# Optimization experiments

Hardware: AMD Instinct MI355X
Metric: run time of the kernel (lower is better)

## Reference

```python
import jax, jax.numpy as jnp
import numpy as np

H = 2048        # hidden_size
NH = 16         # query heads
NKV = 4         # kv heads (= NH//4, from k_proj shape H x H//4)
HD = H // NH    # head_dim = 128
B, S = 2, 2048
SCALE = 1.0 / (HD ** 0.5)


def _rope(x, cos, sin):
    # x: [B, h, S, d]; cos/sin: [S, d//2]; rotate complex pairs (even, odd)
    xr = x[..., 0::2]
    xi = x[..., 1::2]
    c = cos[None, None, :x.shape[2], :]
    s = sin[None, None, :x.shape[2], :]
    out_r = xr * c - xi * s
    out_i = xr * s + xi * c
    return jnp.stack([out_r, out_i], axis=-1).reshape(x.shape)


def setup_inputs() -> dict:
    key = jax.random.key(0)
    ks = jax.random.split(key, 6)
    hidden_states = jax.random.normal(ks[0], (B, S, H), dtype=jnp.float32)
    # RoPE table (theta = 10000), head_dim//2 frequencies
    inv_freq = 1.0 / (10000.0 ** (np.arange(0, HD, 2, dtype=np.float32) / HD))
    angles = np.arange(S, dtype=np.float32)[:, None] * inv_freq[None, :]
    freqs_cos = jnp.asarray(np.cos(angles), dtype=jnp.float32)
    freqs_sin = jnp.asarray(np.sin(angles), dtype=jnp.float32)
    w = 0.02  # keep activations in a sane range
    Wq = jax.random.normal(ks[1], (H, H), dtype=jnp.float32) * w
    Wk = jax.random.normal(ks[2], (H // 4, H), dtype=jnp.float32) * w
    Wv = jax.random.normal(ks[3], (H // 4, H), dtype=jnp.float32) * w
    Wo = jax.random.normal(ks[4], (H, H), dtype=jnp.float32) * w
    return {"hidden_states": hidden_states, "freqs_cos": freqs_cos,
            "freqs_sin": freqs_sin, "Wq": Wq, "Wk": Wk, "Wv": Wv, "Wo": Wo}


def reference(hidden_states, freqs_cos, freqs_sin, Wq, Wk, Wv, Wo):
    b, s, _ = hidden_states.shape
    q = hidden_states @ Wq.T                      # [B,S,H]
    k = hidden_states @ Wk.T                      # [B,S,H/4]
    v = hidden_states @ Wv.T                      # [B,S,H/4]
    q = q.reshape(b, s, NH, HD).transpose(0, 2, 1, 3)    # [B,NH,S,HD]
    k = k.reshape(b, s, NKV, HD).transpose(0, 2, 1, 3)   # [B,NKV,S,HD]
    v = v.reshape(b, s, NKV, HD).transpose(0, 2, 1, 3)
    q = _rope(q, freqs_cos, freqs_sin)
    k = _rope(k, freqs_cos, freqs_sin)
    # GQA: each kv head serves NH//NKV query heads
    k_rep = jnp.repeat(k, NH // NKV, axis=1)      # [B,NH,S,HD]
    v_rep = jnp.repeat(v, NH // NKV, axis=1)
    scores = jnp.einsum('bhqd,bhkd->bhqk', q, k_rep) * SCALE  # [B,NH,S,S]
    probs = jax.nn.softmax(scores, axis=-1)
    out = jnp.einsum('bhqk,bhkd->bhqd', probs, v_rep)         # [B,NH,S,HD]
    out = out.transpose(0, 2, 1, 3).reshape(b, s, H)
    return out @ Wo.T
```

## Files before the change

kernel.cpp:

```cpp
#include <hip/hip_runtime.h>

typedef __bf16 bf16_t;
typedef bf16_t bf16x8 __attribute__((ext_vector_type(8)));
typedef bf16_t bf16x4 __attribute__((ext_vector_type(4)));
typedef bf16_t bf16x2 __attribute__((ext_vector_type(2)));
typedef float f32x4 __attribute__((ext_vector_type(4)));
typedef float f32x16 __attribute__((ext_vector_type(16)));
typedef unsigned int u32x4 __attribute__((ext_vector_type(4)));

typedef const __attribute__((address_space(1))) void* as1_cvp;
typedef __attribute__((address_space(3))) void* as3_vp;

__device__ __forceinline__ void gload16(const void* g, void* l) {
  __builtin_amdgcn_global_load_lds((as1_cvp)g, (as3_vp)l, 16, 0, 0);
}

__device__ __forceinline__ unsigned pxor32(unsigned x) {
  return (unsigned)__shfl_xor((int)x, 32);
}

__global__ __launch_bounds__(256) void cvt_kernel(const float* __restrict__ src,
                                                  bf16_t* __restrict__ dst, int n8) {
  int i = blockIdx.x * 256 + threadIdx.x;
  if (i >= n8) return;
  int idx = i * 8;
  float4 a = *(const float4*)(src + idx);
  float4 b = *(const float4*)(src + idx + 4);
  bf16x8 o;
  o[0] = (bf16_t)a.x; o[1] = (bf16_t)a.y; o[2] = (bf16_t)a.z; o[3] = (bf16_t)a.w;
  o[4] = (bf16_t)b.x; o[5] = (bf16_t)b.y; o[6] = (bf16_t)b.z; o[7] = (bf16_t)b.w;
  *(bf16x8*)(dst + idx) = o;
}

#define BM 128
#define BN 128
#define BK 64

__global__ __launch_bounds__(256, 2) void gemm_bt(const bf16_t* __restrict__ A,
                                                  const bf16_t* __restrict__ B,
                                                  float* __restrict__ C,
                                                  int M, int N, int K) {
  __shared__ alignas(16) bf16_t As[BM * BK];
  __shared__ alignas(16) bf16_t Bs[BN * BK];
  const int t = threadIdx.x;
  const int lane = t & 63, w = t >> 6;
  const int wm = w >> 1, wn = w & 1;
  const int lr = lane & 15, lg = lane >> 4;
  const int m0 = blockIdx.y * BM, n0 = blockIdx.x * BN;
  const int srow = t >> 3, scol = (t & 7) * 8;

  f32x4 acc[4][4] = {};

  for (int kb = 0; kb < K; kb += BK) {
    __syncthreads();
#pragma unroll
    for (int i = 0; i < 4; ++i) {
      gload16(A + (size_t)(m0 + srow + 32 * i) * K + kb + scol, As + i * 2048 + t * 8);
      gload16(B + (size_t)(n0 + srow + 32 * i) * K + kb + scol, Bs + i * 2048 + t * 8);
    }
    __syncthreads();
#pragma unroll
    for (int kk = 0; kk < 2; ++kk) {
      const int ko = kk * 32 + lg * 8;
      bf16x8 af[4], bfr[4];
#pragma unroll
      for (int r = 0; r < 4; ++r)
        af[r] = *(const bf16x8*)(As + (wm * 64 + r * 16 + lr) * BK + ko);
#pragma unroll
      for (int c = 0; c < 4; ++c)
        bfr[c] = *(const bf16x8*)(Bs + (wn * 64 + c * 16 + lr) * BK + ko);
#pragma unroll
      for (int r = 0; r < 4; ++r)
#pragma unroll
        for (int c = 0; c < 4; ++c)
          acc[r][c] = __builtin_amdgcn_mfma_f32_16x16x32_bf16(af[r], bfr[c], acc[r][c], 0, 0, 0);
    }
  }
#pragma unroll
  for (int r = 0; r < 4; ++r)
#pragma unroll
    for (int c = 0; c < 4; ++c)
#pragma unroll
      for (int b = 0; b < 4; ++b)
        C[(size_t)(m0 + wm * 64 + r * 16 + lg * 4 + b) * N + n0 + wn * 64 + c * 16 + lr] =
            acc[r][c][b];
}

__global__ __launch_bounds__(256, 2) void gemm_qkv(const bf16_t* __restrict__ A,
                                                   const bf16_t* __restrict__ B,
                                                   const float* __restrict__ cs,
                                                   const float* __restrict__ sn,
                                                   bf16_t* __restrict__ qr,
                                                   bf16_t* __restrict__ kr,
                                                   bf16_t* __restrict__ vt) {
  __shared__ alignas(16) bf16_t As[BM * BK];
  __shared__ alignas(16) bf16_t Bs[BN * BK];
  const int K = 2048;
  const int t = threadIdx.x;
  const int lane = t & 63, w = t >> 6;
  const int wm = w >> 1, wn = w & 1;
  const int lr = lane & 15, lg = lane >> 4;
  const int m0 = blockIdx.y * BM, n0 = blockIdx.x * BN;
  const int srow = t >> 3, scol = (t & 7) * 8;

  f32x4 acc[4][4] = {};

  for (int kb = 0; kb < K; kb += BK) {
    __syncthreads();
#pragma unroll
    for (int i = 0; i < 4; ++i) {
      gload16(A + (size_t)(m0 + srow + 32 * i) * K + kb + scol, As + i * 2048 + t * 8);
      gload16(B + (size_t)(n0 + srow + 32 * i) * K + kb + scol, Bs + i * 2048 + t * 8);
    }
    __syncthreads();
#pragma unroll
    for (int kk = 0; kk < 2; ++kk) {
      const int ko = kk * 32 + lg * 8;
      bf16x8 af[4], bfr[4];
#pragma unroll
      for (int r = 0; r < 4; ++r)
        af[r] = *(const bf16x8*)(As + (wm * 64 + r * 16 + lr) * BK + ko);
#pragma unroll
      for (int c = 0; c < 4; ++c)
        bfr[c] = *(const bf16x8*)(Bs + (wn * 64 + c * 16 + lr) * BK + ko);
#pragma unroll
      for (int r = 0; r < 4; ++r)
#pragma unroll
        for (int c = 0; c < 4; ++c)
          acc[r][c] = __builtin_amdgcn_mfma_f32_16x16x32_bf16(af[r], bfr[c], acc[r][c], 0, 0, 0);
    }
  }

  const int head = n0 >> 7;
  const int bb2 = m0 >> 11;
  const int sbase = (m0 & 2047) + wm * 64 + lg * 4;
  if (head < 20) {
    bf16_t* dst = (head < 16) ? qr + (size_t)(bb2 * 16 + head) * 2048 * 128
                              : kr + (size_t)(bb2 * 4 + (head - 16)) * 2048 * 128;
    const bool evn = (lr & 1) == 0;
#pragma unroll
    for (int r = 0; r < 4; ++r)
#pragma unroll
      for (int c = 0; c < 4; ++c) {
        const int cw = wn * 64 + c * 16 + lr;
        const int dix = cw >> 1;
#pragma unroll
        for (int b = 0; b < 4; ++b) {
          const int s = sbase + r * 16 + b;
          float own = acc[r][c][b];
          float prt = __shfl_xor(own, 1);
          if (evn) {
            float cc = cs[s * 64 + dix];
            float ssn = sn[s * 64 + dix];
            bf16x2 pr;
            pr[0] = (bf16_t)(own * cc - prt * ssn);
            pr[1] = (bf16_t)(own * ssn + prt * cc);
            *(bf16x2*)(dst + (size_t)s * 128 + cw) = pr;
          }
        }
      }
  } else {
    bf16_t* dst = vt + (size_t)(bb2 * 4 + (head - 20)) * 128 * 2048;
#pragma unroll
    for (int r = 0; r < 4; ++r)
#pragma unroll
      for (int c = 0; c < 4; ++c) {
        const int cw = wn * 64 + c * 16 + lr;
        const int s = sbase + r * 16;
        bf16x4 v4;
#pragma unroll
        for (int b = 0; b < 4; ++b) v4[b] = (bf16_t)acc[r][c][b];
        *(bf16x4*)(dst + (size_t)cw * 2048 + s) = v4;
      }
  }
}

#define KVB 64
__global__ __launch_bounds__(256, 2) void attn_kernel(const bf16_t* __restrict__ Q,
                                                      const bf16_t* __restrict__ Kg,
                                                      const bf16_t* __restrict__ Vg,
                                                      bf16_t* __restrict__ O) {
  __shared__ alignas(16) bf16_t Ks[2][16 * KVB * 8];
  __shared__ alignas(16) bf16_t Vs[8 * 128 * 8];
  const int t = threadIdx.x;
  const int lane = t & 63, w = t >> 6;
  const int l31 = lane & 31, hi = lane >> 5;
  const int bid = ((blockIdx.x & 7) << 6) | (blockIdx.x >> 3);
  const int qt = bid & 15;
  const int h = (bid >> 4) & 15;
  const int bb = bid >> 8;
  const int kvh = h >> 2;

  const bf16_t* Qh = Q + (((size_t)bb * 16 + h) * 2048 + qt * 128 + w * 32) * 128;
  const bf16_t* Kh = Kg + ((size_t)bb * 4 + kvh) * 2048 * 128;
  const bf16_t* Vh = Vg + ((size_t)bb * 4 + kvh) * 128 * 2048;

  bf16x8 qf[8];
#pragma unroll
  for (int c = 0; c < 8; ++c)
    qf[c] = *(const bf16x8*)(Qh + l31 * 128 + c * 16 + hi * 8);

  f32x16 o[4] = {};
  float m2 = -1e30f;
  float ls = 0.f;
  const float sm = 0.08838834764831845f * 1.44269504088896f;

#define STAGE_K(buf, kb)                                                                \
  _Pragma("unroll") for (int i = 0; i < 4; ++i)                                         \
    gload16(Kh + (size_t)((kb) + (t & 63)) * 128 + (i * 4 + (t >> 6)) * 8,              \
            &Ks[buf][(i * 256 + t) * 8]);
#define STAGE_V(kb)                                                                     \
  _Pragma("unroll") for (int i = 0; i < 4; ++i)                                         \
    gload16(Vh + (size_t)(t & 127) * 2048 + (kb) + (i * 2 + (t >> 7)) * 8,              \
            &Vs[(i * 256 + t) * 8]);

  STAGE_K(0, 0);
  __syncthreads();

  for (int tt = 0; tt < 32; ++tt) {
    const int cur = tt & 1;
    STAGE_V(tt * KVB);
    if (tt < 31) { STAGE_K(cur ^ 1, (tt + 1) * KVB); }
    const bf16_t* Kc = Ks[cur];

    f32x16 s0 = {}, s1 = {};
    __builtin_amdgcn_s_setprio(1);
#pragma unroll
    for (int c = 0; c < 8; ++c) {
      bf16x8 kf0 = *(const bf16x8*)(Kc + ((c * 2 + hi) * 64 + l31) * 8);
      bf16x8 kf1 = *(const bf16x8*)(Kc + ((c * 2 + hi) * 64 + 32 + l31) * 8);
      s0 = __builtin_amdgcn_mfma_f32_32x32x16_bf16(kf0, qf[c], s0, 0, 0, 0);
      s1 = __builtin_amdgcn_mfma_f32_32x32x16_bf16(kf1, qf[c], s1, 0, 0, 0);
    }
    __builtin_amdgcn_s_setprio(0);
    s0 = s0 * sm;
    s1 = s1 * sm;

    float tm[8];
#pragma unroll
    for (int j = 0; j < 8; ++j)
      tm[j] = fmaxf(fmaxf(s0[2 * j], s0[2 * j + 1]), fmaxf(s1[2 * j], s1[2 * j + 1]));
    float mx = fmaxf(fmaxf(fmaxf(tm[0], tm[1]), fmaxf(tm[2], tm[3])),
                     fmaxf(fmaxf(tm[4], tm[5]), fmaxf(tm[6], tm[7])));
    mx = fmaxf(mx, __shfl_xor(mx, 32));

    if (__any(mx > m2 + 8.0f)) {
      float mn = fmaxf(m2, mx);
      float resc = exp2f(m2 - mn);
      m2 = mn;
      ls *= resc;
      float rf[16];
#pragma unroll
      for (int r = 0; r < 16; ++r) rf[r] = __shfl(resc, (r & 3) + 8 * (r >> 2) + 4 * hi);
#pragma unroll
      for (int dblk = 0; dblk < 4; ++dblk)
#pragma unroll
        for (int r = 0; r < 16; ++r) o[dblk][r] *= rf[r];
    }
#pragma unroll
    for (int r = 0; r < 16; ++r) {
      float p0 = exp2f(s0[r] - m2);
      float p1 = exp2f(s1[r] - m2);
      s0[r] = p0; s1[r] = p1;
      ls += p0 + p1;
    }

    unsigned Wa[8], Wb[8];
#pragma unroll
    for (int s = 0; s < 8; ++s) {
      bf16x2 a = {(bf16_t)s0[2 * s], (bf16_t)s0[2 * s + 1]};
      bf16x2 b = {(bf16_t)s1[2 * s], (bf16_t)s1[2 * s + 1]};
      Wa[s] = __builtin_bit_cast(unsigned, a);
      Wb[s] = __builtin_bit_cast(unsigned, b);
    }
    bf16x8 pf[4];
    {
      unsigned wv[16];
#pragma unroll
      for (int g = 0; g < 4; ++g) {
        unsigned* W = (g & 2) ? Wb : Wa;
        const int o4 = (g & 1) * 4;
        unsigned pp0 = pxor32(W[o4 + 0]);
        unsigned pp1 = pxor32(W[o4 + 1]);
        unsigned pp2 = pxor32(W[o4 + 2]);
        unsigned pp3 = pxor32(W[o4 + 3]);
        wv[g * 4 + 0] = hi ? pp2 : W[o4 + 0];
        wv[g * 4 + 1] = hi ? pp3 : W[o4 + 1];
        wv[g * 4 + 2] = hi ? W[o4 + 2] : pp0;
        wv[g * 4 + 3] = hi ? W[o4 + 3] : pp1;
      }
      u32x4 pw0 = {wv[0], wv[1], wv[2], wv[3]};
      u32x4 pw1 = {wv[4], wv[5], wv[6], wv[7]};
      u32x4 pw2 = {wv[8], wv[9], wv[10], wv[11]};
      u32x4 pw3 = {wv[12], wv[13], wv[14], wv[15]};
      pf[0] = __builtin_bit_cast(bf16x8, pw0);
      pf[1] = __builtin_bit_cast(bf16x8, pw1);
      pf[2] = __builtin_bit_cast(bf16x8, pw2);
      pf[3] = __builtin_bit_cast(bf16x8, pw3);
    }

    __syncthreads();

    __builtin_amdgcn_s_setprio(1);
#pragma unroll
    for (int kk = 0; kk < 4; ++kk) {
#pragma unroll
      for (int dblk = 0; dblk < 4; ++dblk) {
        bf16x8 vf = *(const bf16x8*)(Vs + ((kk * 2 + hi) * 128 + dblk * 32 + l31) * 8);
        o[dblk] = __builtin_amdgcn_mfma_f32_32x32x16_bf16(pf[kk], vf, o[dblk], 0, 0, 0);
      }
    }
    __builtin_amdgcn_s_setprio(0);
    __syncthreads();
  }

  float lt = ls + __shfl_xor(ls, 32);
  float rinv = 1.0f / lt;
  float rq[16];
#pragma unroll
  for (int r = 0; r < 16; ++r) rq[r] = __shfl(rinv, (r & 3) + 8 * (r >> 2) + 4 * hi);
  const size_t q0 = (size_t)bb * 2048 + qt * 128 + w * 32;
#pragma unroll
  for (int dblk = 0; dblk < 4; ++dblk)
#pragma unroll
    for (int r = 0; r < 16; ++r) {
      const int qrow = (r & 3) + 8 * (r >> 2) + 4 * hi;
      O[(q0 + qrow) * 2048 + h * 128 + dblk * 32 + l31] = (bf16_t)(o[dblk][r] * rq[r]);
    }
}

extern "C" void kernel_launch(void* const* d_in, const int* in_sizes, int n_in,
                              void* d_out, int out_size, void* d_ws, size_t ws_size,
                              hipStream_t stream) {
  const float* hs = (const float*)d_in[0];
  const float* fc = (const float*)d_in[1];
  const float* fs = (const float*)d_in[2];
  const float* Wq = (const float*)d_in[3];
  const float* Wk = (const float*)d_in[4];
  const float* Wv = (const float*)d_in[5];
  const float* Wo = (const float*)d_in[6];
  float* out = (float*)d_out;

  char* ws = (char*)d_ws;
  bf16_t* hs_b = (bf16_t*)ws;
  bf16_t* wcat = (bf16_t*)(ws + 16777216);
  bf16_t* wo_b = (bf16_t*)(ws + 29360128);
  bf16_t* qr = (bf16_t*)(ws + 37748736);
  bf16_t* kr = (bf16_t*)(ws + 54525952);
  bf16_t* vt = (bf16_t*)(ws + 58720256);
  bf16_t* ao = (bf16_t*)(ws + 62914560);

  cvt_kernel<<<8388608 / 8 / 256, 256, 0, stream>>>(hs, hs_b, 8388608 / 8);
  cvt_kernel<<<4194304 / 8 / 256, 256, 0, stream>>>(Wq, wcat, 4194304 / 8);
  cvt_kernel<<<1048576 / 8 / 256, 256, 0, stream>>>(Wk, wcat + 4194304, 1048576 / 8);
  cvt_kernel<<<1048576 / 8 / 256, 256, 0, stream>>>(Wv, wcat + 5242880, 1048576 / 8);
  cvt_kernel<<<4194304 / 8 / 256, 256, 0, stream>>>(Wo, wo_b, 4194304 / 8);

  dim3 g1(3072 / BN, 4096 / BM);
  gemm_qkv<<<g1, 256, 0, stream>>>(hs_b, wcat, fc, fs, qr, kr, vt);

  attn_kernel<<<512, 256, 0, stream>>>(qr, kr, vt, ao);

  dim3 g2(2048 / BN, 4096 / BM);
  gemm_bt<<<g2, 256, 0, stream>>>(ao, wo_b, out, 4096, 2048, 2048);
}
```

Measured before the change: 246.4 us.

## Split attention KV range in two halves with combine kernel, merge conversions

The attention kernel now splits each query tile's KV sequence into two halves, doubling the grid from 512 to 1024 blocks. Each half writes partial normalized outputs plus the running max and sum, and a new combine kernel merges them into the attention output. The five fp32-to-bf16 conversion launches are merged into one kernel, and the softmax scale is folded into an fma inside exp2. The extra blocks give better CU occupancy on a 256-CU part, at the cost of extra partial-output traffic and one more launch.

Result: slower. 254.4 us (+3.3%).

```diff
diff --git a/kernel.cpp b/kernel.cpp
--- a/kernel.cpp
+++ b/kernel.cpp
@@ -19,17 +19,34 @@
   return (unsigned)__shfl_xor((int)x, 32);
 }
 
-__global__ __launch_bounds__(256) void cvt_kernel(const float* __restrict__ src,
-                                                  bf16_t* __restrict__ dst, int n8) {
+__global__ __launch_bounds__(256) void cvtall_kernel(const float* __restrict__ hs,
+                                                     const float* __restrict__ Wq,
+                                                     const float* __restrict__ Wk,
+                                                     const float* __restrict__ Wv,
+                                                     const float* __restrict__ Wo,
+                                                     bf16_t* __restrict__ hs_b,
+                                                     bf16_t* __restrict__ wcat,
+                                                     bf16_t* __restrict__ wo_b) {
   int i = blockIdx.x * 256 + threadIdx.x;
-  if (i >= n8) return;
-  int idx = i * 8;
-  float4 a = *(const float4*)(src + idx);
-  float4 b = *(const float4*)(src + idx + 4);
+  const float* s;
+  bf16_t* d;
+  if (i < 1048576) {
+    s = hs + (size_t)i * 8;            d = hs_b + (size_t)i * 8;
+  } else if (i < 1572864) {
+    int j = i - 1048576; s = Wq + (size_t)j * 8; d = wcat + (size_t)j * 8;
+  } else if (i < 1703936) {
+    int j = i - 1572864; s = Wk + (size_t)j * 8; d = wcat + 4194304 + (size_t)j * 8;
+  } else if (i < 1835008) {
+    int j = i - 1703936; s = Wv + (size_t)j * 8; d = wcat + 5242880 + (size_t)j * 8;
+  } else {
+    int j = i - 1835008; s = Wo + (size_t)j * 8; d = wo_b + (size_t)j * 8;
+  }
+  float4 a = *(const float4*)s;
+  float4 b = *(const float4*)(s + 4);
   bf16x8 o;
   o[0] = (bf16_t)a.x; o[1] = (bf16_t)a.y; o[2] = (bf16_t)a.z; o[3] = (bf16_t)a.w;
   o[4] = (bf16_t)b.x; o[5] = (bf16_t)b.y; o[6] = (bf16_t)b.z; o[7] = (bf16_t)b.w;
-  *(bf16x8*)(dst + idx) = o;
+  *(bf16x8*)d = o;
 }
 
 #define BM 128
@@ -179,21 +196,23 @@
 __global__ __launch_bounds__(256, 2) void attn_kernel(const bf16_t* __restrict__ Q,
                                                       const bf16_t* __restrict__ Kg,
                                                       const bf16_t* __restrict__ Vg,
-                                                      bf16_t* __restrict__ O) {
+                                                      bf16_t* __restrict__ OP,
+                                                      float* __restrict__ ML) {
   __shared__ alignas(16) bf16_t Ks[2][16 * KVB * 8];
   __shared__ alignas(16) bf16_t Vs[8 * 128 * 8];
   const int t = threadIdx.x;
   const int lane = t & 63, w = t >> 6;
   const int l31 = lane & 31, hi = lane >> 5;
-  const int bid = ((blockIdx.x & 7) << 6) | (blockIdx.x >> 3);
+  const int bid = ((blockIdx.x & 7) << 7) | (blockIdx.x >> 3);
   const int qt = bid & 15;
   const int h = (bid >> 4) & 15;
-  const int bb = bid >> 8;
+  const int bb = (bid >> 8) & 1;
+  const int half = bid >> 9;
   const int kvh = h >> 2;
 
   const bf16_t* Qh = Q + (((size_t)bb * 16 + h) * 2048 + qt * 128 + w * 32) * 128;
-  const bf16_t* Kh = Kg + ((size_t)bb * 4 + kvh) * 2048 * 128;
-  const bf16_t* Vh = Vg + ((size_t)bb * 4 + kvh) * 128 * 2048;
+  const bf16_t* Kh = Kg + (((size_t)bb * 4 + kvh) * 2048 + half * 1024) * 128;
+  const bf16_t* Vh = Vg + ((size_t)bb * 4 + kvh) * 128 * 2048 + half * 1024;
 
   bf16x8 qf[8];
 #pragma unroll
@@ -217,10 +236,10 @@
   STAGE_K(0, 0);
   __syncthreads();
 
-  for (int tt = 0; tt < 32; ++tt) {
+  for (int tt = 0; tt < 16; ++tt) {
     const int cur = tt & 1;
     STAGE_V(tt * KVB);
-    if (tt < 31) { STAGE_K(cur ^ 1, (tt + 1) * KVB); }
+    if (tt < 15) { STAGE_K(cur ^ 1, (tt + 1) * KVB); }
     const bf16_t* Kc = Ks[cur];
 
     f32x16 s0 = {}, s1 = {};
@@ -233,16 +252,15 @@
       s1 = __builtin_amdgcn_mfma_f32_32x32x16_bf16(kf1, qf[c], s1, 0, 0, 0);
     }
     __builtin_amdgcn_s_setprio(0);
-    s0 = s0 * sm;
-    s1 = s1 * sm;
 
     float tm[8];
 #pragma unroll
     for (int j = 0; j < 8; ++j)
       tm[j] = fmaxf(fmaxf(s0[2 * j], s0[2 * j + 1]), fmaxf(s1[2 * j], s1[2 * j + 1]));
-    float mx = fmaxf(fmaxf(fmaxf(tm[0], tm[1]), fmaxf(tm[2], tm[3])),
-                     fmaxf(fmaxf(tm[4], tm[5]), fmaxf(tm[6], tm[7])));
-    mx = fmaxf(mx, __shfl_xor(mx, 32));
+    float mxr = fmaxf(fmaxf(fmaxf(tm[0], tm[1]), fmaxf(tm[2], tm[3])),
+                      fmaxf(fmaxf(tm[4], tm[5]), fmaxf(tm[6], tm[7])));
+    mxr = fmaxf(mxr, __shfl_xor(mxr, 32));
+    float mx = mxr * sm;
 
     if (__any(mx > m2 + 8.0f)) {
       float mn = fmaxf(m2, mx);
@@ -259,8 +277,8 @@
     }
 #pragma unroll
     for (int r = 0; r < 16; ++r) {
-      float p0 = exp2f(s0[r] - m2);
-      float p1 = exp2f(s1[r] - m2);
+      float p0 = exp2f(fmaf(s0[r], sm, -m2));
+      float p1 = exp2f(fmaf(s1[r], sm, -m2));
       s0[r] = p0; s1[r] = p1;
       ls += p0 + p1;
     }
@@ -320,13 +338,44 @@
 #pragma unroll
   for (int r = 0; r < 16; ++r) rq[r] = __shfl(rinv, (r & 3) + 8 * (r >> 2) + 4 * hi);
   const size_t q0 = (size_t)bb * 2048 + qt * 128 + w * 32;
+  bf16_t* Od = OP + (size_t)half * 4096 * 2048;
 #pragma unroll
   for (int dblk = 0; dblk < 4; ++dblk)
 #pragma unroll
     for (int r = 0; r < 16; ++r) {
       const int qrow = (r & 3) + 8 * (r >> 2) + 4 * hi;
-      O[(q0 + qrow) * 2048 + h * 128 + dblk * 32 + l31] = (bf16_t)(o[dblk][r] * rq[r]);
-    }
+      Od[(q0 + qrow) * 2048 + h * 128 + dblk * 32 + l31] = (bf16_t)(o[dblk][r] * rq[r]);
+    }
+  if (hi == 0) {
+    const size_t mlrow = (size_t)half * 65536 + ((size_t)bb * 16 + h) * 2048
+                       + qt * 128 + w * 32 + l31;
+    ML[mlrow * 2] = m2;
+    ML[mlrow * 2 + 1] = lt;
+  }
+}
+
+__global__ __launch_bounds__(256) void comb_kernel(const bf16_t* __restrict__ OP,
+                                                   const float* __restrict__ ML,
+                                                   bf16_t* __restrict__ ao) {
+  int idx = blockIdx.x * 256 + threadIdx.x;
+  int r = idx >> 8;
+  int col = (idx & 255) * 8;
+  int h = col >> 7;
+  int bb = r >> 11, s = r & 2047;
+  size_t mlrow = ((size_t)bb * 16 + h) * 2048 + s;
+  float m0 = ML[mlrow * 2],             l0 = ML[mlrow * 2 + 1];
+  float m1 = ML[(65536 + mlrow) * 2],   l1 = ML[(65536 + mlrow) * 2 + 1];
+  float mm = fmaxf(m0, m1);
+  float w0 = l0 * exp2f(m0 - mm), w1 = l1 * exp2f(m1 - mm);
+  float inv = 1.0f / (w0 + w1);
+  w0 *= inv; w1 *= inv;
+  bf16x8 a = *(const bf16x8*)(OP + (size_t)r * 2048 + col);
+  bf16x8 b = *(const bf16x8*)(OP + (size_t)4096 * 2048 + (size_t)r * 2048 + col);
+  bf16x8 o;
+#pragma unroll
+  for (int j = 0; j < 8; ++j)
+    o[j] = (bf16_t)(w0 * (float)a[j] + w1 * (float)b[j]);
+  *(bf16x8*)(ao + (size_t)r * 2048 + col) = o;
 }
 
 extern "C" void kernel_launch(void* const* d_in, const int* in_sizes, int n_in,
@@ -349,17 +398,16 @@
   bf16_t* kr = (bf16_t*)(ws + 54525952);
   bf16_t* vt = (bf16_t*)(ws + 58720256);
   bf16_t* ao = (bf16_t*)(ws + 62914560);
-
-  cvt_kernel<<<8388608 / 8 / 256, 256, 0, stream>>>(hs, hs_b, 8388608 / 8);
-  cvt_kernel<<<4194304 / 8 / 256, 256, 0, stream>>>(Wq, wcat, 4194304 / 8);
-  cvt_kernel<<<1048576 / 8 / 256, 256, 0, stream>>>(Wk, wcat + 4194304, 1048576 / 8);
-  cvt_kernel<<<1048576 / 8 / 256, 256, 0, stream>>>(Wv, wcat + 5242880, 1048576 / 8);
-  cvt_kernel<<<4194304 / 8 / 256, 256, 0, stream>>>(Wo, wo_b, 4194304 / 8);
+  bf16_t* opart = (bf16_t*)(ws + 79691776);
+  float*  ml = (float*)(ws + 113246208);
+
+  cvtall_kernel<<<9216, 256, 0, stream>>>(hs, Wq, Wk, Wv, Wo, hs_b, wcat, wo_b);
 
   dim3 g1(3072 / BN, 4096 / BM);
   gemm_qkv<<<g1, 256, 0, stream>>>(hs_b, wcat, fc, fs, qr, kr, vt);
 
-  attn_kernel<<<512, 256, 0, stream>>>(qr, kr, vt, ao);
+  attn_kernel<<<1024, 256, 0, stream>>>(qr, kr, vt, opart, ml);
+  comb_kernel<<<4096, 256, 0, stream>>>(opart, ml, ao);
 
   dim3 g2(2048 / BN, 4096 / BM);
   gemm_bt<<<g2, 256, 0, stream>>>(ao, wo_b, out, 4096, 2048, 2048);
```
